# Kernel tuning notes

Measured on AMD Instinct MI355X. Metric: run time of the kernel, lower is better.

Reference implementation:

```python
import jax, jax.numpy as jnp
import numpy as np

T, B, C, S = 4096, 8, 512, 2048


def setup_inputs() -> dict:
    key = jax.random.key(0)
    k1, k2, k3 = jax.random.split(key, 3)
    x = jax.random.normal(k1, (T, B, C), dtype=jnp.float32)
    downsampling_mask = jax.random.uniform(k2, (B, T, S), dtype=jnp.float32)
    size_of_groups = jax.random.randint(k3, (B, S), 0, 4, dtype=jnp.int64)
    leftmost_group = jnp.zeros((1, 1, C), dtype=jnp.float32)
    return {"x": x, "downsampling_mask": downsampling_mask,
            "size_of_groups": size_of_groups, "leftmost_group": leftmost_group}


def reference(x, downsampling_mask, size_of_groups, leftmost_group):
    # mode == 'average': masked grouped pooling as a dense contraction
    # x: [T,B,C], mask: [B,T,S] -> downsampled: [S,B,C]
    downsampled = jnp.einsum('tbc,bts->sbc', x, downsampling_mask)
    # prepend learned leftmost group embedding, broadcast over batch
    left = jnp.broadcast_to(leftmost_group, (1, x.shape[1], x.shape[2]))
    return jnp.concatenate([left, downsampled], axis=0)  # [S+1, B, C]
```

## Files before the change

kernel.cpp:

```cpp
#include <hip/hip_runtime.h>
#include <hip/hip_bf16.h>

constexpr int T  = 4096;
constexpr int Bb = 8;
constexpr int C  = 512;
constexpr int S  = 2048;
constexpr int BC = Bb * C;

constexpr int BK = 32;
constexpr int NK = T / BK;

typedef __bf16 bf16x8 __attribute__((ext_vector_type(8)));
typedef float  f32x16 __attribute__((ext_vector_type(16)));
typedef float  f32x4  __attribute__((ext_vector_type(4)));

__device__ inline unsigned pk2(float lo, float hi) {
    union { __hip_bfloat16 h; unsigned short u; } a, b;
    a.h = __float2bfloat16(lo);
    b.h = __float2bfloat16(hi);
    return ((unsigned)b.u << 16) | (unsigned)a.u;
}

__device__ inline int slot16(int s) { return s ^ ((s >> 2) & 7); }

__global__ void left_fill(const float* __restrict__ left, float* __restrict__ out) {
    int i = blockIdx.x * blockDim.x + threadIdx.x;
    if (i < BC) out[i] = left[i & (C - 1)];
}

__global__ __launch_bounds__(256, 4) void ds_gemm(
    const float* __restrict__ x,
    const float* __restrict__ mask,
    float* __restrict__ out)
{
    __shared__ __align__(16) unsigned char smem[32768];

    const int bid = blockIdx.x;
    const int mt  = bid & 15;
    const int nt  = (bid >> 4) & 3;
    const int b   = bid >> 6;

    const int tid  = threadIdx.x;
    const int lane = tid & 63;
    const int wave = tid >> 6;
    const int wm = wave >> 1;
    const int wn = wave & 1;
    const int lm = lane & 31;
    const int kg = lane >> 5;

    const int  ii  = tid & 127;
    const int  sg  = ii & 31;
    const int  tg  = ii >> 5;
    const bool stB = (tid >= 128);

    const float* gsrc = stB
        ? x    + (size_t)(tg * 8) * BC + b * C + nt * 128 + sg * 4
        : mask + (size_t)b * T * S + (size_t)(tg * 8) * S + mt * 128 + sg * 4;
    const size_t grow  = stB ? (size_t)BC : (size_t)S;
    const size_t gstep = grow * BK;

    int waddr[4];
#pragma unroll
    for (int j = 0; j < 4; ++j)
        waddr[j] = (stB ? 8192 : 0) + tg * 2048 + slot16(sg * 4 + j) * 16;

    int raddrA[2][2], raddrB[2][2];
#pragma unroll
    for (int kk = 0; kk < 2; ++kk)
#pragma unroll
        for (int q = 0; q < 2; ++q) {
            raddrA[kk][q] = (kk * 2 + kg) * 2048 + slot16(wm * 64 + q * 32 + lm) * 16;
            raddrB[kk][q] = 8192 + (kk * 2 + kg) * 2048 + slot16(wn * 64 + q * 32 + lm) * 16;
        }

    f32x16 acc[2][2] = {};
    f32x4  L[8];

#define LOAD_TILE(k)                                                        \
    {                                                                       \
        const float* p_ = gsrc + (size_t)(k) * gstep;                       \
        _Pragma("unroll") for (int r = 0; r < 8; ++r)                       \
            L[r] = *(const f32x4*)(p_ + (size_t)r * grow);                  \
    }

#define WRITE_TILE(buf)                                                     \
    {                                                                       \
        const int boff_ = (buf) * 16384;                                    \
        _Pragma("unroll") for (int j = 0; j < 4; ++j) {                     \
            uint4 w_;                                                       \
            w_.x = pk2(L[0][j], L[1][j]);                                   \
            w_.y = pk2(L[2][j], L[3][j]);                                   \
            w_.z = pk2(L[4][j], L[5][j]);                                   \
            w_.w = pk2(L[6][j], L[7][j]);                                   \
            *(uint4*)(smem + boff_ + waddr[j]) = w_;                        \
        }                                                                   \
    }

#define COMPUTE(buf)                                                        \
    {                                                                       \
        const int boff_ = (buf) * 16384;                                    \
        _Pragma("unroll") for (int kk = 0; kk < 2; ++kk) {                  \
            bf16x8 a0_ = *(const bf16x8*)(smem + boff_ + raddrA[kk][0]);    \
            bf16x8 a1_ = *(const bf16x8*)(smem + boff_ + raddrA[kk][1]);    \
            bf16x8 b0_ = *(const bf16x8*)(smem + boff_ + raddrB[kk][0]);    \
            bf16x8 b1_ = *(const bf16x8*)(smem + boff_ + raddrB[kk][1]);    \
            acc[0][0] = __builtin_amdgcn_mfma_f32_32x32x16_bf16(a0_, b0_, acc[0][0], 0, 0, 0); \
            acc[0][1] = __builtin_amdgcn_mfma_f32_32x32x16_bf16(a0_, b1_, acc[0][1], 0, 0, 0); \
            acc[1][0] = __builtin_amdgcn_mfma_f32_32x32x16_bf16(a1_, b0_, acc[1][0], 0, 0, 0); \
            acc[1][1] = __builtin_amdgcn_mfma_f32_32x32x16_bf16(a1_, b1_, acc[1][1], 0, 0, 0); \
        }                                                                   \
    }

    LOAD_TILE(0);

    for (int k = 0; k < NK; ++k) {
        WRITE_TILE(k & 1);
        if (k + 1 < NK) LOAD_TILE(k + 1);
        __syncthreads();
        COMPUTE(k & 1);
    }

#undef LOAD_TILE
#undef WRITE_TILE
#undef COMPUTE

    const int s_w = mt * 128 + wm * 64;
    const int c_w = nt * 128 + wn * 64;
    float* outp = out + BC;
#pragma unroll
    for (int m2 = 0; m2 < 2; ++m2) {
#pragma unroll
        for (int n2 = 0; n2 < 2; ++n2) {
#pragma unroll
            for (int r = 0; r < 16; ++r) {
                const int row  = (r & 3) + 8 * (r >> 2) + 4 * kg;
                const int srow = s_w + m2 * 32 + row;
                const int ccol = c_w + n2 * 32 + lm;
                outp[(size_t)srow * BC + b * C + ccol] = acc[m2][n2][r];
            }
        }
    }
}

extern "C" void kernel_launch(void* const* d_in, const int* in_sizes, int n_in,
                              void* d_out, int out_size, void* d_ws, size_t ws_size,
                              hipStream_t stream) {
    const float* x    = (const float*)d_in[0];
    const float* mask = (const float*)d_in[1];
    const float* left = (const float*)d_in[3];
    float* out = (float*)d_out;

    left_fill<<<BC / 256, 256, 0, stream>>>(left, out);
    ds_gemm<<<Bb * (S / 128) * (C / 128), 256, 0, stream>>>(x, mask, out);
}
```

Measured before the change: 157.9 us.

## Double block to 512 threads with split-K across wave halves and LDS reduction

```diff
diff --git a/kernel.cpp b/kernel.cpp
--- a/kernel.cpp
+++ b/kernel.cpp
@@ -7,7 +7,7 @@
 constexpr int S  = 2048;
 constexpr int BC = Bb * C;
 
-constexpr int BK = 32;
+constexpr int BK = 64;
 constexpr int NK = T / BK;
 
 typedef __bf16 bf16x8 __attribute__((ext_vector_type(8)));
@@ -28,12 +28,12 @@
     if (i < BC) out[i] = left[i & (C - 1)];
 }
 
-__global__ __launch_bounds__(256, 4) void ds_gemm(
+__global__ __launch_bounds__(512, 4) void ds_gemm(
     const float* __restrict__ x,
     const float* __restrict__ mask,
     float* __restrict__ out)
 {
-    __shared__ __align__(16) unsigned char smem[32768];
+    __shared__ __align__(16) unsigned char smem[65536];
 
     const int bid = blockIdx.x;
     const int mt  = bid & 15;
@@ -43,15 +43,17 @@
     const int tid  = threadIdx.x;
     const int lane = tid & 63;
     const int wave = tid >> 6;
-    const int wm = wave >> 1;
-    const int wn = wave & 1;
+    const int h    = wave >> 2;
+    const int wq   = wave & 3;
+    const int wm = wq >> 1;
+    const int wn = wq & 1;
     const int lm = lane & 31;
     const int kg = lane >> 5;
 
-    const int  ii  = tid & 127;
+    const int  ii  = tid & 255;
     const int  sg  = ii & 31;
     const int  tg  = ii >> 5;
-    const bool stB = (tid >= 128);
+    const bool stB = (tid >= 256);
 
     const float* gsrc = stB
         ? x    + (size_t)(tg * 8) * BC + b * C + nt * 128 + sg * 4
@@ -62,15 +64,16 @@
     int waddr[4];
 #pragma unroll
     for (int j = 0; j < 4; ++j)
-        waddr[j] = (stB ? 8192 : 0) + tg * 2048 + slot16(sg * 4 + j) * 16;
+        waddr[j] = (stB ? 16384 : 0) + tg * 2048 + slot16(sg * 4 + j) * 16;
 
     int raddrA[2][2], raddrB[2][2];
 #pragma unroll
     for (int kk = 0; kk < 2; ++kk)
 #pragma unroll
         for (int q = 0; q < 2; ++q) {
-            raddrA[kk][q] = (kk * 2 + kg) * 2048 + slot16(wm * 64 + q * 32 + lm) * 16;
-            raddrB[kk][q] = 8192 + (kk * 2 + kg) * 2048 + slot16(wn * 64 + q * 32 + lm) * 16;
+            const int oct = h * 4 + kk * 2 + kg;
+            raddrA[kk][q] = oct * 2048 + slot16(wm * 64 + q * 32 + lm) * 16;
+            raddrB[kk][q] = 16384 + oct * 2048 + slot16(wn * 64 + q * 32 + lm) * 16;
         }
 
     f32x16 acc[2][2] = {};
@@ -85,7 +88,7 @@
 
 #define WRITE_TILE(buf)                                                     \
     {                                                                       \
-        const int boff_ = (buf) * 16384;                                    \
+        const int boff_ = (buf) * 32768;                                    \
         _Pragma("unroll") for (int j = 0; j < 4; ++j) {                     \
             uint4 w_;                                                       \
             w_.x = pk2(L[0][j], L[1][j]);                                   \
@@ -98,7 +101,7 @@
 
 #define COMPUTE(buf)                                                        \
     {                                                                       \
-        const int boff_ = (buf) * 16384;                                    \
+        const int boff_ = (buf) * 32768;                                    \
         _Pragma("unroll") for (int kk = 0; kk < 2; ++kk) {                  \
             bf16x8 a0_ = *(const bf16x8*)(smem + boff_ + raddrA[kk][0]);    \
             bf16x8 a1_ = *(const bf16x8*)(smem + boff_ + raddrA[kk][1]);    \
@@ -124,21 +127,50 @@
 #undef WRITE_TILE
 #undef COMPUTE
 
-    const int s_w = mt * 128 + wm * 64;
-    const int c_w = nt * 128 + wn * 64;
-    float* outp = out + BC;
+    __syncthreads();
+    if (h == 1) {
 #pragma unroll
-    for (int m2 = 0; m2 < 2; ++m2) {
+        for (int m2 = 0; m2 < 2; ++m2)
 #pragma unroll
-        for (int n2 = 0; n2 < 2; ++n2) {
+            for (int n2 = 0; n2 < 2; ++n2) {
+                unsigned char* base = smem + (wave - 4) * 16384 + (m2 * 2 + n2) * 4096 + lane * 16;
 #pragma unroll
-            for (int r = 0; r < 16; ++r) {
-                const int row  = (r & 3) + 8 * (r >> 2) + 4 * kg;
-                const int srow = s_w + m2 * 32 + row;
-                const int ccol = c_w + n2 * 32 + lm;
-                outp[(size_t)srow * BC + b * C + ccol] = acc[m2][n2][r];
+                for (int r4 = 0; r4 < 4; ++r4) {
+                    f32x4 v = { acc[m2][n2][r4 * 4 + 0], acc[m2][n2][r4 * 4 + 1],
+                                acc[m2][n2][r4 * 4 + 2], acc[m2][n2][r4 * 4 + 3] };
+                    *(f32x4*)(base + r4 * 1024) = v;
+                }
             }
-        }
+    }
+    __syncthreads();
+    if (h == 0) {
+#pragma unroll
+        for (int m2 = 0; m2 < 2; ++m2)
+#pragma unroll
+            for (int n2 = 0; n2 < 2; ++n2) {
+                const unsigned char* base = smem + wave * 16384 + (m2 * 2 + n2) * 4096 + lane * 16;
+#pragma unroll
+                for (int r4 = 0; r4 < 4; ++r4) {
+                    f32x4 v = *(const f32x4*)(base + r4 * 1024);
+#pragma unroll
+                    for (int j = 0; j < 4; ++j) acc[m2][n2][r4 * 4 + j] += v[j];
+                }
+            }
+
+        const int s_w = mt * 128 + wm * 64;
+        const int c_w = nt * 128 + wn * 64;
+        float* outp = out + BC;
+#pragma unroll
+        for (int m2 = 0; m2 < 2; ++m2)
+#pragma unroll
+            for (int n2 = 0; n2 < 2; ++n2)
+#pragma unroll
+                for (int r = 0; r < 16; ++r) {
+                    const int row  = (r & 3) + 8 * (r >> 2) + 4 * kg;
+                    const int srow = s_w + m2 * 32 + row;
+                    const int ccol = c_w + n2 * 32 + lm;
+                    outp[(size_t)srow * BC + b * C + ccol] = acc[m2][n2][r];
+                }
     }
 }
 
@@ -151,5 +183,5 @@
     float* out = (float*)d_out;
 
     left_fill<<<BC / 256, 256, 0, stream>>>(left, out);
-    ds_gemm<<<Bb * (S / 128) * (C / 128), 256, 0, stream>>>(x, mask, out);
+    ds_gemm<<<Bb * (S / 128) * (C / 128), 512, 0, stream>>>(x, mask, out);
 }
```

After: 163.0 us. 1.03x slower.

## Enlarge GEMM tile to 256x128 with 512 threads, triple-buffered LDS and XCD-aware mapping

Applied to the files above, without the earlier changes.

```diff
diff --git a/kernel.cpp b/kernel.cpp
--- a/kernel.cpp
+++ b/kernel.cpp
@@ -28,17 +28,19 @@
     if (i < BC) out[i] = left[i & (C - 1)];
 }
 
-__global__ __launch_bounds__(256, 4) void ds_gemm(
+__global__ __launch_bounds__(512, 2) void ds_gemm(
     const float* __restrict__ x,
     const float* __restrict__ mask,
     float* __restrict__ out)
 {
-    __shared__ __align__(16) unsigned char smem[32768];
+    __shared__ __align__(16) unsigned char smem[73728];
 
-    const int bid = blockIdx.x;
-    const int mt  = bid & 15;
-    const int nt  = (bid >> 4) & 3;
-    const int b   = bid >> 6;
+    const int bid0 = blockIdx.x;
+    const int xcd  = bid0 & 7;
+    const int slot = bid0 >> 3;
+    const int b    = xcd;
+    const int mt   = slot & 7;
+    const int nt   = slot >> 3;
 
     const int tid  = threadIdx.x;
     const int lane = tid & 63;
@@ -48,57 +50,59 @@
     const int lm = lane & 31;
     const int kg = lane >> 5;
 
-    const int  ii  = tid & 127;
-    const int  sg  = ii & 31;
-    const int  tg  = ii >> 5;
-    const bool stB = (tid >= 128);
+    const bool stA = (tid < 256);
+    const bool stB = (tid >= 256 && tid < 384);
+    const int  ii  = stA ? tid : (tid - 256);
+    const int  sg  = stA ? (ii & 63) : (ii & 31);
+    const int  tg  = stA ? (ii >> 6) : (ii >> 5);
 
-    const float* gsrc = stB
-        ? x    + (size_t)(tg * 8) * BC + b * C + nt * 128 + sg * 4
-        : mask + (size_t)b * T * S + (size_t)(tg * 8) * S + mt * 128 + sg * 4;
-    const size_t grow  = stB ? (size_t)BC : (size_t)S;
+    const float* gsrc = stA
+        ? mask + (size_t)b * T * S + (size_t)(tg * 8) * S + mt * 256 + sg * 4
+        : x    + (size_t)(tg * 8) * BC + b * C + nt * 128 + sg * 4;
+    const size_t grow  = stA ? (size_t)S : (size_t)BC;
     const size_t gstep = grow * BK;
 
     int waddr[4];
 #pragma unroll
     for (int j = 0; j < 4; ++j)
-        waddr[j] = (stB ? 8192 : 0) + tg * 2048 + slot16(sg * 4 + j) * 16;
+        waddr[j] = stA ? (tg * 4096 + slot16(sg * 4 + j) * 16)
+                       : (16384 + tg * 2048 + slot16(sg * 4 + j) * 16);
 
     int raddrA[2][2], raddrB[2][2];
 #pragma unroll
     for (int kk = 0; kk < 2; ++kk)
 #pragma unroll
         for (int q = 0; q < 2; ++q) {
-            raddrA[kk][q] = (kk * 2 + kg) * 2048 + slot16(wm * 64 + q * 32 + lm) * 16;
-            raddrB[kk][q] = 8192 + (kk * 2 + kg) * 2048 + slot16(wn * 64 + q * 32 + lm) * 16;
+            raddrA[kk][q] = (kk * 2 + kg) * 4096 + slot16(wm * 64 + q * 32 + lm) * 16;
+            raddrB[kk][q] = 16384 + (kk * 2 + kg) * 2048 + slot16(wn * 64 + q * 32 + lm) * 16;
         }
 
     f32x16 acc[2][2] = {};
-    f32x4  L[8];
+    f32x4  L0[8], L1[8];
 
-#define LOAD_TILE(k)                                                        \
-    {                                                                       \
+#define LOAD_TILE(Lr, k)                                                    \
+    if (stA || stB) {                                                       \
         const float* p_ = gsrc + (size_t)(k) * gstep;                       \
         _Pragma("unroll") for (int r = 0; r < 8; ++r)                       \
-            L[r] = *(const f32x4*)(p_ + (size_t)r * grow);                  \
+            Lr[r] = *(const f32x4*)(p_ + (size_t)r * grow);                 \
     }
 
-#define WRITE_TILE(buf)                                                     \
-    {                                                                       \
-        const int boff_ = (buf) * 16384;                                    \
+#define WRITE_TILE(Lr, buf)                                                 \
+    if (stA || stB) {                                                       \
+        const int boff_ = (buf) * 24576;                                    \
         _Pragma("unroll") for (int j = 0; j < 4; ++j) {                     \
             uint4 w_;                                                       \
-            w_.x = pk2(L[0][j], L[1][j]);                                   \
-            w_.y = pk2(L[2][j], L[3][j]);                                   \
-            w_.z = pk2(L[4][j], L[5][j]);                                   \
-            w_.w = pk2(L[6][j], L[7][j]);                                   \
+            w_.x = pk2(Lr[0][j], Lr[1][j]);                                 \
+            w_.y = pk2(Lr[2][j], Lr[3][j]);                                 \
+            w_.z = pk2(Lr[4][j], Lr[5][j]);                                 \
+            w_.w = pk2(Lr[6][j], Lr[7][j]);                                 \
             *(uint4*)(smem + boff_ + waddr[j]) = w_;                        \
         }                                                                   \
     }
 
 #define COMPUTE(buf)                                                        \
     {                                                                       \
-        const int boff_ = (buf) * 16384;                                    \
+        const int boff_ = (buf) * 24576;                                    \
         _Pragma("unroll") for (int kk = 0; kk < 2; ++kk) {                  \
             bf16x8 a0_ = *(const bf16x8*)(smem + boff_ + raddrA[kk][0]);    \
             bf16x8 a1_ = *(const bf16x8*)(smem + boff_ + raddrA[kk][1]);    \
@@ -111,26 +115,33 @@
         }                                                                   \
     }
 
-    LOAD_TILE(0);
+    LOAD_TILE(L0, 0);
+    LOAD_TILE(L1, 1);
 
     for (int k = 0; k < NK; ++k) {
-        WRITE_TILE(k & 1);
-        if (k + 1 < NK) LOAD_TILE(k + 1);
+        const int buf = k % 3;
+        if (k & 1) {
+            WRITE_TILE(L1, buf);
+            if (k + 2 < NK) LOAD_TILE(L1, k + 2);
+        } else {
+            WRITE_TILE(L0, buf);
+            if (k + 2 < NK) LOAD_TILE(L0, k + 2);
+        }
         __syncthreads();
-        COMPUTE(k & 1);
+        COMPUTE(buf);
     }
 
 #undef LOAD_TILE
 #undef WRITE_TILE
 #undef COMPUTE
 
-    const int s_w = mt * 128 + wm * 64;
+    const int s_w = mt * 256 + wm * 64;
     const int c_w = nt * 128 + wn * 64;
     float* outp = out + BC;
 #pragma unroll
-    for (int m2 = 0; m2 < 2; ++m2) {
+    for (int m2 = 0; m2 < 2; ++m2)
 #pragma unroll
-        for (int n2 = 0; n2 < 2; ++n2) {
+        for (int n2 = 0; n2 < 2; ++n2)
 #pragma unroll
             for (int r = 0; r < 16; ++r) {
                 const int row  = (r & 3) + 8 * (r >> 2) + 4 * kg;
@@ -138,8 +149,6 @@
                 const int ccol = c_w + n2 * 32 + lm;
                 outp[(size_t)srow * BC + b * C + ccol] = acc[m2][n2][r];
             }
-        }
-    }
 }
 
 extern "C" void kernel_launch(void* const* d_in, const int* in_sizes, int n_in,
@@ -151,5 +160,5 @@
     float* out = (float*)d_out;
 
     left_fill<<<BC / 256, 256, 0, stream>>>(left, out);
-    ds_gemm<<<Bb * (S / 128) * (C / 128), 256, 0, stream>>>(x, mask, out);
+    ds_gemm<<<Bb * (S / 256) * (C / 128), 512, 0, stream>>>(x, mask, out);
 }
```

Result: slower. 214.1 us (+35.6%).
